# Kernel optimization log

Hardware: AMD Instinct MI355X
Metric: run time of the kernel (lower is better)

## Reference

```python
import jax, jax.numpy as jnp
import numpy as np

B, T, C = 2, 4096, 768
H = 12
D = C // H  # head_dim = 64


def setup_inputs() -> dict:
    key = jax.random.key(0)
    kx, kq, kk, kv, ko = jax.random.split(key, 5)
    s = 1.0 / np.sqrt(C)  # keep activations well-scaled
    return {
        "x": jax.random.normal(kx, (B, T, C), dtype=jnp.float32),
        "wq": jax.random.normal(kq, (C, C), dtype=jnp.float32) * s,
        "wk": jax.random.normal(kk, (C, C), dtype=jnp.float32) * s,
        "wv": jax.random.normal(kv, (C, C), dtype=jnp.float32) * s,
        "wo": jax.random.normal(ko, (C, C), dtype=jnp.float32) * s,
    }


def reference(x, wq, wk, wv, wo):
    b, t, c = x.shape
    # projections (torch Linear: y = x @ W.T); split heads -> (B,H,T,D)
    q = (x @ wq.T).reshape(b, t, H, D).transpose(0, 2, 1, 3)
    k = (x @ wk.T).reshape(b, t, H, D).transpose(0, 2, 1, 3)
    v = (x @ wv.T).reshape(b, t, H, D).transpose(0, 2, 1, 3)
    scale = 1.0 / jnp.sqrt(jnp.asarray(D, dtype=x.dtype))
    scores = jnp.einsum("bhqd,bhkd->bhqk", q, k) * scale  # (B,H,T,T)
    causal = jnp.tril(jnp.ones((t, t), dtype=bool))
    scores = jnp.where(causal, scores, jnp.asarray(-jnp.inf, dtype=scores.dtype))
    attn = jax.nn.softmax(scores, axis=-1)
    ctx = jnp.einsum("bhqk,bhkd->bhqd", attn, v)  # (B,H,T,D)
    ctx = ctx.transpose(0, 2, 1, 3).reshape(b, t, c)
    return ctx @ wo.T
```

## Files before the change

kernel.cpp:

```cpp
#include <hip/hip_runtime.h>
#include <hip/hip_bf16.h>

#define B_  2
#define T_  4096
#define C_  768
#define H_  12
#define D_  64
#define MTOT (B_*T_)

typedef __bf16 bf16;
typedef __bf16 bf16x8 __attribute__((ext_vector_type(8)));
typedef __bf16 bf16x4 __attribute__((ext_vector_type(4)));
typedef float  f32x4  __attribute__((ext_vector_type(4)));
typedef unsigned int u32x4 __attribute__((ext_vector_type(4)));

__device__ __forceinline__ void gl_lds16(const bf16* g, bf16* l) {
    __builtin_amdgcn_global_load_lds(
        (const __attribute__((address_space(1))) void*)g,
        (__attribute__((address_space(3))) void*)l, 16, 0, 0);
}

__device__ __forceinline__ void pswap32_16(unsigned int& x, unsigned int& y) {
    auto r1 = __builtin_amdgcn_permlane32_swap(x, y, false, false);
    auto r2 = __builtin_amdgcn_permlane16_swap(r1[0], r1[1], false, false);
    x = r2[0]; y = r2[1];
}
__device__ __forceinline__ unsigned int cvtpk(float lo, float hi) {
    unsigned int r;
    asm("v_cvt_pk_bf16_f32 %0, %1, %2" : "=v"(r) : "v"(lo), "v"(hi));
    return r;
}

__global__ __launch_bounds__(256) void cvt_bf16(const float* __restrict__ src,
                                                bf16* __restrict__ dst, int n8) {
    int i = blockIdx.x * 256 + threadIdx.x;
    if (i >= n8) return;
    const float4* s4 = (const float4*)src;
    float4 a = s4[2*(size_t)i], b = s4[2*(size_t)i+1];
    bf16x8 o;
    o[0]=(bf16)a.x; o[1]=(bf16)a.y; o[2]=(bf16)a.z; o[3]=(bf16)a.w;
    o[4]=(bf16)b.x; o[5]=(bf16)b.y; o[6]=(bf16)b.z; o[7]=(bf16)b.w;
    *(bf16x8*)(dst + 8*(size_t)i) = o;
}

__global__ __launch_bounds__(256) void cvt_bf16_w4(const float* __restrict__ w0,
                                                   const float* __restrict__ w1,
                                                   const float* __restrict__ w2,
                                                   const float* __restrict__ w3,
                                                   bf16* __restrict__ d0,
                                                   bf16* __restrict__ d1,
                                                   bf16* __restrict__ d2,
                                                   bf16* __restrict__ d3) {
    int z = blockIdx.y;
    const float* src = (z==0)?w0:(z==1)?w1:(z==2)?w2:w3;
    bf16* dst = (z==0)?d0:(z==1)?d1:(z==2)?d2:d3;
    int i = blockIdx.x * 256 + threadIdx.x;
    const float4* s4 = (const float4*)src;
    float4 a = s4[2*(size_t)i], b = s4[2*(size_t)i+1];
    bf16x8 o;
    o[0]=(bf16)a.x; o[1]=(bf16)a.y; o[2]=(bf16)a.z; o[3]=(bf16)a.w;
    o[4]=(bf16)b.x; o[5]=(bf16)b.y; o[6]=(bf16)b.z; o[7]=(bf16)b.w;
    *(bf16x8*)(dst + 8*(size_t)i) = o;
}

__global__ __launch_bounds__(256) void gemm_qkv(const bf16* __restrict__ xb,
                                                const bf16* __restrict__ wqb,
                                                const bf16* __restrict__ wkb,
                                                const bf16* __restrict__ wvb,
                                                bf16* __restrict__ qo,
                                                bf16* __restrict__ ko,
                                                bf16* __restrict__ vto) {
    int z = blockIdx.z;
    const bf16* w = (z == 0) ? wqb : (z == 1) ? wkb : wvb;
    bf16* dst = (z == 0) ? qo : (z == 1) ? ko : vto;
    int mbase = blockIdx.x * 128;
    int nbase = blockIdx.y * 128;
    __shared__ bf16 As[128][32];
    __shared__ bf16 Bs[128][32];
    int tid  = threadIdx.x;
    int wave = tid >> 6, lane = tid & 63;
    int wm = (wave >> 1) * 64, wn = (wave & 1) * 64;
    int lr = lane & 15, lg = lane >> 4;
    int srow0 = tid >> 2, scol0 = tid & 3;
    int srow1 = (tid + 256) >> 2, scol1 = (tid + 256) & 3;
    f32x4 acc[4][4] = {};
    for (int kb = 0; kb < C_; kb += 32) {
        gl_lds16(xb + (size_t)(mbase + srow0) * C_ + kb + scol0 * 8, &As[srow0][scol0 * 8]);
        gl_lds16(xb + (size_t)(mbase + srow1) * C_ + kb + scol1 * 8, &As[srow1][scol1 * 8]);
        gl_lds16(w  + (size_t)(nbase + srow0) * C_ + kb + scol0 * 8, &Bs[srow0][scol0 * 8]);
        gl_lds16(w  + (size_t)(nbase + srow1) * C_ + kb + scol1 * 8, &Bs[srow1][scol1 * 8]);
        __syncthreads();
        bf16x8 af[4], bfr[4];
        #pragma unroll
        for (int mt = 0; mt < 4; ++mt) af[mt]  = *(const bf16x8*)(&As[wm + mt*16 + lr][lg*8]);
        #pragma unroll
        for (int nt = 0; nt < 4; ++nt) bfr[nt] = *(const bf16x8*)(&Bs[wn + nt*16 + lr][lg*8]);
        #pragma unroll
        for (int mt = 0; mt < 4; ++mt)
            #pragma unroll
            for (int nt = 0; nt < 4; ++nt)
                acc[mt][nt] = __builtin_amdgcn_mfma_f32_16x16x32_bf16(af[mt], bfr[nt], acc[mt][nt], 0, 0, 0);
        __syncthreads();
    }
    float sc = (z == 0) ? 0.18033688011112042f : 1.0f;
    int m0 = mbase + wm + (lg << 2);
    int n0 = nbase + wn + lr;
    if (z < 2) {
        #pragma unroll
        for (int mt = 0; mt < 4; ++mt) {
            #pragma unroll
            for (int nt = 0; nt < 4; ++nt) {
                int n = n0 + nt * 16;
                int h = n >> 6, d = n & 63;
                #pragma unroll
                for (int r = 0; r < 4; ++r) {
                    int m = m0 + mt * 16 + r;
                    int b = m >> 12, t = m & 4095;
                    dst[(((size_t)b * H_ + h) * T_ + t) * 64 + d] = (bf16)(acc[mt][nt][r] * sc);
                }
            }
        }
    } else {
        #pragma unroll
        for (int mt = 0; mt < 4; ++mt) {
            int m = m0 + mt * 16;
            int b = m >> 12, t = m & 4095;
            #pragma unroll
            for (int nt = 0; nt < 4; ++nt) {
                int n = n0 + nt * 16;
                int h = n >> 6, d = n & 63;
                bf16x4 pk;
                #pragma unroll
                for (int r = 0; r < 4; ++r) pk[r] = (bf16)acc[mt][nt][r];
                *(bf16x4*)(dst + (((size_t)b * H_ + h) * 64 + d) * T_ + t) = pk;
            }
        }
    }
}

__global__ __launch_bounds__(256) void gemm_out(const bf16* __restrict__ ctx,
                                                const bf16* __restrict__ wob,
                                                float* __restrict__ out) {
    int mbase = blockIdx.x * 128;
    int nbase = blockIdx.y * 128;
    __shared__ bf16 As[128][32];
    __shared__ bf16 Bs[128][32];
    int tid  = threadIdx.x;
    int wave = tid >> 6, lane = tid & 63;
    int wm = (wave >> 1) * 64, wn = (wave & 1) * 64;
    int lr = lane & 15, lg = lane >> 4;
    int srow0 = tid >> 2, scol0 = tid & 3;
    int srow1 = (tid + 256) >> 2, scol1 = (tid + 256) & 3;
    f32x4 acc[4][4] = {};
    for (int kb = 0; kb < C_; kb += 32) {
        gl_lds16(ctx + (size_t)(mbase + srow0) * C_ + kb + scol0 * 8, &As[srow0][scol0 * 8]);
        gl_lds16(ctx + (size_t)(mbase + srow1) * C_ + kb + scol1 * 8, &As[srow1][scol1 * 8]);
        gl_lds16(wob + (size_t)(nbase + srow0) * C_ + kb + scol0 * 8, &Bs[srow0][scol0 * 8]);
        gl_lds16(wob + (size_t)(nbase + srow1) * C_ + kb + scol1 * 8, &Bs[srow1][scol1 * 8]);
        __syncthreads();
        bf16x8 af[4], bfr[4];
        #pragma unroll
        for (int mt = 0; mt < 4; ++mt) af[mt]  = *(const bf16x8*)(&As[wm + mt*16 + lr][lg*8]);
        #pragma unroll
        for (int nt = 0; nt < 4; ++nt) bfr[nt] = *(const bf16x8*)(&Bs[wn + nt*16 + lr][lg*8]);
        #pragma unroll
        for (int mt = 0; mt < 4; ++mt)
            #pragma unroll
            for (int nt = 0; nt < 4; ++nt)
                acc[mt][nt] = __builtin_amdgcn_mfma_f32_16x16x32_bf16(af[mt], bfr[nt], acc[mt][nt], 0, 0, 0);
        __syncthreads();
    }
    int m0 = mbase + wm + (lg << 2);
    int n0 = nbase + wn + lr;
    #pragma unroll
    for (int mt = 0; mt < 4; ++mt)
        #pragma unroll
        for (int nt = 0; nt < 4; ++nt)
            #pragma unroll
            for (int r = 0; r < 4; ++r)
                out[(size_t)(m0 + mt * 16 + r) * C_ + n0 + nt * 16] = acc[mt][nt][r];
}

__device__ __forceinline__ void attn_store(const f32x4 (&o)[4], float l, bf16* __restrict__ ctx,
                                           int b, int qrow, int h, int lg) {
    float inv = 1.0f / l;
    #pragma unroll
    for (int dt = 0; dt < 4; ++dt) {
        bf16x4 pk;
        #pragma unroll
        for (int r = 0; r < 4; ++r) pk[r] = (bf16)(o[dt][r] * inv);
        *(bf16x4*)(ctx + ((size_t)b * T_ + qrow) * C_ + h * 64 + dt * 16 + lg * 4) = pk;
    }
}

__global__ __launch_bounds__(256) void attn(const bf16* __restrict__ q,
                                            const bf16* __restrict__ k,
                                            const bf16* __restrict__ vt,
                                            bf16* __restrict__ ctx) {
    int idx = blockIdx.x;
    int qt = 63 - idx / 24;
    int bh = idx % 24;
    int b = bh / H_, h = bh % H_;
    int tid = threadIdx.x;
    int wave = tid >> 6, lane = tid & 63;
    int lr = lane & 15, lg = lane >> 4;

    __shared__ bf16 Ks[64][72];
    __shared__ bf16 Vs[64][72];

    const bf16* qp = q  + (size_t)bh * T_ * 64;
    const bf16* kp = k  + (size_t)bh * T_ * 64;
    const bf16* vp = vt + (size_t)bh * 64 * (size_t)T_;

    int r0 = tid >> 3, c0 = tid & 7;
    const bf16* kstg = kp + (size_t)r0 * 64 + c0 * 8;
    const bf16* vstg = vp + (size_t)r0 * T_ + c0 * 8;

    const float NEGINF = -__builtin_inff();

    int qb = qt * 64 + wave * 16;
    int n  = qt + 1;
    int qrow = qb + lr;

    bf16x8 qf[2];
    #pragma unroll
    for (int c = 0; c < 2; ++c)
        qf[c] = *(const bf16x8*)(qp + (size_t)(qb + lr) * 64 + c * 32 + lg * 8);

    f32x4 o[4] = {};
    float lsum = 0.f;
    const f32x4 fz = {};

    uint4 sk0 = *(const uint4*)(kstg);
    uint4 sk1 = *(const uint4*)(kstg + 32 * 64);
    uint4 sv0 = *(const uint4*)(vstg);
    uint4 sv1 = *(const uint4*)(vstg + (size_t)32 * T_);

    for (int kb = 0; kb < n; ++kb) {
        int kv = kb * 64;
        __syncthreads();
        *(uint4*)(&Ks[r0][c0 * 8])      = sk0;
        *(uint4*)(&Ks[32 + r0][c0 * 8]) = sk1;
        *(uint4*)(&Vs[r0][c0 * 8])      = sv0;
        *(uint4*)(&Vs[32 + r0][c0 * 8]) = sv1;
        if (kb + 1 < n) {
            const bf16* ksrc = kstg + (size_t)(kb + 1) * 64 * 64;
            const bf16* vsrc = vstg + (size_t)(kb + 1) * 64;
            sk0 = *(const uint4*)(ksrc);
            sk1 = *(const uint4*)(ksrc + 32 * 64);
            sv0 = *(const uint4*)(vsrc);
            sv1 = *(const uint4*)(vsrc + (size_t)32 * T_);
        }
        __syncthreads();

        f32x4 s[4];
        __builtin_amdgcn_s_setprio(1);
        #pragma unroll
        for (int nt = 0; nt < 4; ++nt) {
            bf16x8 kf0 = *(const bf16x8*)(&Ks[nt * 16 + lr][lg * 8]);
            s[nt] = __builtin_amdgcn_mfma_f32_16x16x32_bf16(kf0, qf[0], fz, 0, 0, 0);
        }
        #pragma unroll
        for (int nt = 0; nt < 4; ++nt) {
            bf16x8 kf1 = *(const bf16x8*)(&Ks[nt * 16 + lr][32 + lg * 8]);
            s[nt] = __builtin_amdgcn_mfma_f32_16x16x32_bf16(kf1, qf[1], s[nt], 0, 0, 0);
        }
        __builtin_amdgcn_s_setprio(0);
        if (kb == qt) {
            #pragma unroll
            for (int nt = 0; nt < 4; ++nt)
                #pragma unroll
                for (int r = 0; r < 4; ++r) {
                    int key = kv + nt * 16 + lg * 4 + r;
                    s[nt][r] = (key > qrow) ? NEGINF : s[nt][r];
                }
        }
        #pragma unroll
        for (int nt = 0; nt < 4; ++nt) {
            #pragma unroll
            for (int r = 0; r < 4; ++r)
                s[nt][r] = __builtin_amdgcn_exp2f(s[nt][r]);
            lsum += (s[nt][0] + s[nt][1]) + (s[nt][2] + s[nt][3]);
        }
        unsigned int dpk[8];
        #pragma unroll
        for (int nt = 0; nt < 4; ++nt) {
            dpk[2*nt]   = cvtpk(s[nt][0], s[nt][1]);
            dpk[2*nt+1] = cvtpk(s[nt][2], s[nt][3]);
        }
        unsigned int pw[2][4];
        #pragma unroll
        for (int c2 = 0; c2 < 2; ++c2)
            #pragma unroll
            for (int pr = 0; pr < 2; ++pr) {
                unsigned int x = dpk[4*c2 + pr], y = dpk[4*c2 + 2 + pr];
                pswap32_16(x, y);
                pw[c2][pr] = x;
                pw[c2][2+pr] = y;
            }
        __builtin_amdgcn_s_setprio(1);
        #pragma unroll
        for (int c2 = 0; c2 < 2; ++c2) {
            u32x4 pt;
            pt[0] = pw[c2][0]; pt[1] = pw[c2][1]; pt[2] = pw[c2][2]; pt[3] = pw[c2][3];
            bf16x8 pf = __builtin_bit_cast(bf16x8, pt);
            #pragma unroll
            for (int dt = 0; dt < 4; ++dt) {
                bf16x8 vfr = *(const bf16x8*)(&Vs[dt * 16 + lr][c2 * 32 + lg * 8]);
                o[dt] = __builtin_amdgcn_mfma_f32_16x16x32_bf16(vfr, pf, o[dt], 0, 0, 0);
            }
        }
        __builtin_amdgcn_s_setprio(0);
    }

    float l = lsum;
    l += __shfl_xor(l, 16, 64);
    l += __shfl_xor(l, 32, 64);
    attn_store(o, l, ctx, b, qrow, h, lg);
}

extern "C" void kernel_launch(void* const* d_in, const int* in_sizes, int n_in,
                              void* d_out, int out_size, void* d_ws, size_t ws_size,
                              hipStream_t stream) {
    const float* x  = (const float*)d_in[0];
    const float* wq = (const float*)d_in[1];
    const float* wk = (const float*)d_in[2];
    const float* wv = (const float*)d_in[3];
    const float* wo = (const float*)d_in[4];
    float* out = (float*)d_out;

    char* ws = (char*)d_ws;
    const size_t SZ_XB = (size_t)MTOT * C_ * sizeof(bf16);
    const size_t SZ_W  = (size_t)C_ * C_ * sizeof(bf16);
    bf16* xb  = (bf16*)(ws);
    bf16* wqb = (bf16*)(ws + SZ_XB);
    bf16* wkb = (bf16*)(ws + SZ_XB + SZ_W);
    bf16* wvb = (bf16*)(ws + SZ_XB + 2 * SZ_W);
    bf16* wob = (bf16*)(ws + SZ_XB + 3 * SZ_W);
    bf16* qb  = (bf16*)(ws + SZ_XB + 4 * SZ_W);
    bf16* kb  = (bf16*)(ws + 2 * SZ_XB + 4 * SZ_W);
    bf16* vtb = (bf16*)(ws + 3 * SZ_XB + 4 * SZ_W);
    bf16* ctb = (bf16*)(ws + 4 * SZ_XB + 4 * SZ_W);

    cvt_bf16<<<3072, 256, 0, stream>>>(x, xb, MTOT * C_ / 8);
    cvt_bf16_w4<<<dim3(288, 4), 256, 0, stream>>>(wq, wk, wv, wo, wqb, wkb, wvb, wob);

    gemm_qkv<<<dim3(MTOT / 128, C_ / 128, 3), 256, 0, stream>>>(xb, wqb, wkb, wvb, qb, kb, vtb);
    attn<<<1536, 256, 0, stream>>>(qb, kb, vtb, ctb);
    gemm_out<<<dim3(MTOT / 128, C_ / 128), 256, 0, stream>>>(ctb, wob, out);
}
```

Measured before the change: 233.9 us.

## Double-buffer attention K/V tiles via direct global-to-LDS loads with XOR swizzle

The attention kernel now stages K and V tiles straight into LDS with global_load_lds into a two-slot buffer, prefetching the next tile while computing on the current one. Padding is dropped in favor of an XOR-swizzled column layout on both the load source and the fragment reads, to avoid bank conflicts. This removes the register round trip and one barrier per iteration, at the cost of doubled LDS use. It relies on the barrier at the end of each iteration to also cover completion of the async loads.

```diff
diff --git a/kernel.cpp b/kernel.cpp
--- a/kernel.cpp
+++ b/kernel.cpp
@@ -205,22 +205,36 @@
     int wave = tid >> 6, lane = tid & 63;
     int lr = lane & 15, lg = lane >> 4;
 
-    __shared__ bf16 Ks[64][72];
-    __shared__ bf16 Vs[64][72];
+    __shared__ bf16 Ks[2][64][64];
+    __shared__ bf16 Vs[2][64][64];
 
     const bf16* qp = q  + (size_t)bh * T_ * 64;
     const bf16* kp = k  + (size_t)bh * T_ * 64;
     const bf16* vp = vt + (size_t)bh * 64 * (size_t)T_;
 
     int r0 = tid >> 3, c0 = tid & 7;
-    const bf16* kstg = kp + (size_t)r0 * 64 + c0 * 8;
-    const bf16* vstg = vp + (size_t)r0 * T_ + c0 * 8;
+    int cs = (c0 ^ (r0 & 7)) * 8;
+    const bf16* kstg = kp + (size_t)r0 * 64 + cs;
+    const bf16* vstg = vp + (size_t)r0 * T_ + cs;
+
+#define STAGE(kb_, cb_) do { \
+        const bf16* ks_ = kstg + (size_t)(kb_) * 64 * 64; \
+        const bf16* vs_ = vstg + (size_t)(kb_) * 64; \
+        gl_lds16(ks_,                   &Ks[cb_][r0][c0 * 8]); \
+        gl_lds16(ks_ + 32 * 64,         &Ks[cb_][32 + r0][c0 * 8]); \
+        gl_lds16(vs_,                   &Vs[cb_][r0][c0 * 8]); \
+        gl_lds16(vs_ + (size_t)32 * T_, &Vs[cb_][32 + r0][c0 * 8]); \
+    } while (0)
 
     const float NEGINF = -__builtin_inff();
 
     int qb = qt * 64 + wave * 16;
     int n  = qt + 1;
     int qrow = qb + lr;
+
+    int sw = lr & 7;
+    int col0 = (lg ^ sw) * 8;
+    int col1 = ((4 | lg) ^ sw) * 8;
 
     bf16x8 qf[2];
     #pragma unroll
@@ -231,38 +245,24 @@
     float lsum = 0.f;
     const f32x4 fz = {};
 
-    uint4 sk0 = *(const uint4*)(kstg);
-    uint4 sk1 = *(const uint4*)(kstg + 32 * 64);
-    uint4 sv0 = *(const uint4*)(vstg);
-    uint4 sv1 = *(const uint4*)(vstg + (size_t)32 * T_);
+    STAGE(0, 0);
+    __syncthreads();
+    int cur = 0;
 
     for (int kb = 0; kb < n; ++kb) {
         int kv = kb * 64;
-        __syncthreads();
-        *(uint4*)(&Ks[r0][c0 * 8])      = sk0;
-        *(uint4*)(&Ks[32 + r0][c0 * 8]) = sk1;
-        *(uint4*)(&Vs[r0][c0 * 8])      = sv0;
-        *(uint4*)(&Vs[32 + r0][c0 * 8]) = sv1;
-        if (kb + 1 < n) {
-            const bf16* ksrc = kstg + (size_t)(kb + 1) * 64 * 64;
-            const bf16* vsrc = vstg + (size_t)(kb + 1) * 64;
-            sk0 = *(const uint4*)(ksrc);
-            sk1 = *(const uint4*)(ksrc + 32 * 64);
-            sv0 = *(const uint4*)(vsrc);
-            sv1 = *(const uint4*)(vsrc + (size_t)32 * T_);
-        }
-        __syncthreads();
+        if (kb + 1 < n) STAGE(kb + 1, cur ^ 1);
 
         f32x4 s[4];
         __builtin_amdgcn_s_setprio(1);
         #pragma unroll
         for (int nt = 0; nt < 4; ++nt) {
-            bf16x8 kf0 = *(const bf16x8*)(&Ks[nt * 16 + lr][lg * 8]);
+            bf16x8 kf0 = *(const bf16x8*)(&Ks[cur][nt * 16 + lr][col0]);
             s[nt] = __builtin_amdgcn_mfma_f32_16x16x32_bf16(kf0, qf[0], fz, 0, 0, 0);
         }
         #pragma unroll
         for (int nt = 0; nt < 4; ++nt) {
-            bf16x8 kf1 = *(const bf16x8*)(&Ks[nt * 16 + lr][32 + lg * 8]);
+            bf16x8 kf1 = *(const bf16x8*)(&Ks[cur][nt * 16 + lr][col1]);
             s[nt] = __builtin_amdgcn_mfma_f32_16x16x32_bf16(kf1, qf[1], s[nt], 0, 0, 0);
         }
         __builtin_amdgcn_s_setprio(0);
@@ -304,14 +304,19 @@
             u32x4 pt;
             pt[0] = pw[c2][0]; pt[1] = pw[c2][1]; pt[2] = pw[c2][2]; pt[3] = pw[c2][3];
             bf16x8 pf = __builtin_bit_cast(bf16x8, pt);
+            int vcol = c2 ? col1 : col0;
             #pragma unroll
             for (int dt = 0; dt < 4; ++dt) {
-                bf16x8 vfr = *(const bf16x8*)(&Vs[dt * 16 + lr][c2 * 32 + lg * 8]);
+                bf16x8 vfr = *(const bf16x8*)(&Vs[cur][dt * 16 + lr][vcol]);
                 o[dt] = __builtin_amdgcn_mfma_f32_16x16x32_bf16(vfr, pf, o[dt], 0, 0, 0);
             }
         }
         __builtin_amdgcn_s_setprio(0);
-    }
+
+        __syncthreads();
+        cur ^= 1;
+    }
+#undef STAGE
 
     float l = lsum;
     l += __shfl_xor(l, 16, 64);
```

Result: faster. 228.9 us (-2.1%).
